# Kernel tuning notes

Hardware: AMD Instinct MI355X
Metric: run time of the kernel (lower is better)

The kernel has to match this reference:

```python
import jax, jax.numpy as jnp
import numpy as np

B, N, D, H, IN, HID = 16, 1024, 256, 8, 256, 1024
HD = IN // H  # head dim = 32
EPS = 1e-5


def layer_norm(x, g, b):
    mu = jnp.mean(x, axis=-1, keepdims=True)
    var = jnp.var(x, axis=-1, keepdims=True)
    return (x - mu) / jnp.sqrt(var + EPS) * g + b


def setup_inputs() -> dict:
    key = jax.random.key(0)
    ks = jax.random.split(key, 12)
    s = 0.02
    return {
        "x": jax.random.normal(ks[0], (B, N, D), jnp.float32),
        "coords": jax.random.normal(ks[1], (B, N, 2), jnp.float32),
        "g1": jnp.ones((D,), jnp.float32),
        "b1": jnp.zeros((D,), jnp.float32),
        "Wqkv": jax.random.normal(ks[2], (3 * IN, D), jnp.float32) * s,
        "Wproj": jax.random.normal(ks[3], (IN, IN), jnp.float32) * s,
        "bproj": jnp.zeros((IN,), jnp.float32),
        "g2": jnp.ones((D,), jnp.float32),
        "b2": jnp.zeros((D,), jnp.float32),
        "W1": jax.random.normal(ks[4], (HID, D), jnp.float32) * s,
        "bb1": jnp.zeros((HID,), jnp.float32),
        "W2": jax.random.normal(ks[5], (D, HID), jnp.float32) * s,
        "bb2": jnp.zeros((D,), jnp.float32),
    }


def reference(x, coords, g1, b1, Wqkv, Wproj, bproj, g2, b2, W1, bb1, W2, bb2):
    # ---- Attention branch (pre-norm) ----
    h = layer_norm(x, g1, b1)                       # [B,N,D]
    qkv = h @ Wqkv.T                                # [B,N,3*IN]
    qkv = qkv.reshape(B, N, 3, H, HD).transpose(2, 0, 3, 1, 4)  # [3,B,H,N,HD]
    q, k, v = qkv[0], qkv[1], qkv[2]
    scale = HD ** -0.5
    attn = jnp.einsum('bhid,bhjd->bhij', q * scale, k)  # [B,H,N,N]
    attn = jax.nn.softmax(attn, axis=-1)
    o = jnp.einsum('bhij,bhjd->bhid', attn, v)      # [B,H,N,HD]
    o = o.transpose(0, 2, 1, 3).reshape(B, N, IN)   # [B,N,IN]
    o = o @ Wproj.T + bproj
    o = o + h                                       # residual inside Attention (vs normed input)
    x = x + o                                       # Block residual (double residual, faithful)
    # ---- MLP branch ----
    h2 = layer_norm(x, g2, b2)
    m = jax.nn.gelu(h2 @ W1.T + bb1, approximate=False) @ W2.T + bb2
    return x + m
```

## Files before the change

kernel.cpp:

```cpp
#include <hip/hip_runtime.h>
#include <hip/hip_bf16.h>
#include <math.h>

#define Bdim 16
#define Ndim 1024
#define Ddim 256
#define Hdim 8
#define HDdim 32
#define INdim 256
#define HIDdim 1024
#define Tdim (Bdim * Ndim)

typedef __attribute__((ext_vector_type(8)))  short bf16x8;
typedef __attribute__((ext_vector_type(4)))  short bf16x4;
typedef __attribute__((ext_vector_type(16))) float f32x16;
typedef unsigned int u32;

__device__ inline short f2bf(float x) {
    union { __hip_bfloat16 b; short s; } u;
    u.b = __float2bfloat16(x);
    return u.s;
}

__device__ inline float bf2f(short s) {
    return __uint_as_float(((u32)(unsigned short)s) << 16);
}

__device__ inline float fexp2(float x) {
#if __has_builtin(__builtin_amdgcn_exp2f)
    return __builtin_amdgcn_exp2f(x);
#else
    return exp2f(x);
#endif
}

__device__ inline u32 pack2bf(float a, float b) {
#if __has_builtin(__builtin_amdgcn_cvt_pk_bf16_f32)
    typedef __attribute__((ext_vector_type(2))) __bf16 bf16x2_t;
    union { bf16x2_t v; u32 u; } c;
    c.v = __builtin_amdgcn_cvt_pk_bf16_f32(a, b);
    return c.u;
#else
    u32 ua = __float_as_uint(a), ub = __float_as_uint(b);
    return ((ua + 0x8000u) >> 16) | ((ub + 0x8000u) & 0xffff0000u);
#endif
}

__device__ inline void plswap(u32 &a, u32 &b) {
    asm volatile("v_permlane32_swap_b32 %0, %1" : "+v"(a), "+v"(b));
}

__device__ inline float gelu_exact(float v) {
    return 0.5f * v * (1.0f + erff(v * 0.70710678118654752f));
}

typedef __attribute__((address_space(1))) const u32 gas_t;
typedef __attribute__((address_space(3))) u32 las_t;
__device__ inline void gl16(const short* g, short* l) {
    __builtin_amdgcn_global_load_lds((gas_t*)g, (las_t*)l, 16, 0, 0);
}

#define N4_QKV  (3 * INdim * Ddim / 4)
#define N4_PROJ (INdim * INdim / 4)
#define N4_W1   (HIDdim * Ddim / 4)
#define N4_W2   (Ddim * HIDdim / 4)
#define NCVT_BLK ((N4_QKV + N4_PROJ + N4_W1 + N4_W2) / 256)

__global__ __launch_bounds__(256) void cvt_ln1_kernel(const float* __restrict__ s0,
                                                      const float* __restrict__ s1,
                                                      const float* __restrict__ s2,
                                                      const float* __restrict__ s3,
                                                      short* __restrict__ d0,
                                                      short* __restrict__ d1,
                                                      short* __restrict__ d2,
                                                      short* __restrict__ d3,
                                                      const float* __restrict__ x,
                                                      const float* __restrict__ g,
                                                      const float* __restrict__ b,
                                                      float* __restrict__ outf,
                                                      short* __restrict__ outb) {
    const int bid = blockIdx.x;
    if (bid < NCVT_BLK) {
        int i = bid * 256 + threadIdx.x;
        const float* src; short* dst; int j;
        if (i < N4_QKV)                          { src = s0; dst = d0; j = i; }
        else if (i < N4_QKV + N4_PROJ)           { src = s1; dst = d1; j = i - N4_QKV; }
        else if (i < N4_QKV + N4_PROJ + N4_W1)   { src = s2; dst = d2; j = i - N4_QKV - N4_PROJ; }
        else                                     { src = s3; dst = d3; j = i - N4_QKV - N4_PROJ - N4_W1; }
        float4 v = ((const float4*)src)[j];
        bf16x4 bb;
        bb[0] = f2bf(v.x); bb[1] = f2bf(v.y); bb[2] = f2bf(v.z); bb[3] = f2bf(v.w);
        ((bf16x4*)dst)[j] = bb;
    } else {
        int w = threadIdx.x >> 6, lane = threadIdx.x & 63;
        int row = (bid - NCVT_BLK) * 4 + w;
        float4 v = ((const float4*)x)[(size_t)row * 64 + lane];
        float s  = (v.x + v.y) + (v.z + v.w);
        float s2 = (v.x * v.x + v.y * v.y) + (v.z * v.z + v.w * v.w);
        #pragma unroll
        for (int off = 32; off; off >>= 1) {
            s  += __shfl_xor(s,  off, 64);
            s2 += __shfl_xor(s2, off, 64);
        }
        float mu   = s * (1.0f / Ddim);
        float var  = s2 * (1.0f / Ddim) - mu * mu;
        float rstd = rsqrtf(var + 1e-5f);
        float4 gg = ((const float4*)g)[lane];
        float4 bb = ((const float4*)b)[lane];
        float4 r;
        r.x = (v.x - mu) * rstd * gg.x + bb.x;
        r.y = (v.y - mu) * rstd * gg.y + bb.y;
        r.z = (v.z - mu) * rstd * gg.z + bb.z;
        r.w = (v.w - mu) * rstd * gg.w + bb.w;
        if (outf) ((float4*)outf)[(size_t)row * 64 + lane] = r;
        bf16x4 rb;
        rb[0] = f2bf(r.x); rb[1] = f2bf(r.y); rb[2] = f2bf(r.z); rb[3] = f2bf(r.w);
        ((bf16x4*)outb)[(size_t)row * 64 + lane] = rb;
    }
}

__global__ __launch_bounds__(256) void ln4_kernel(const float* __restrict__ x,
                                                  const float* __restrict__ g,
                                                  const float* __restrict__ b,
                                                  float* __restrict__ outf,
                                                  short* __restrict__ outb) {
    int w = threadIdx.x >> 6, lane = threadIdx.x & 63;
    int row = blockIdx.x * 4 + w;
    float4 v = ((const float4*)x)[(size_t)row * 64 + lane];
    float s  = (v.x + v.y) + (v.z + v.w);
    float s2 = (v.x * v.x + v.y * v.y) + (v.z * v.z + v.w * v.w);
    #pragma unroll
    for (int off = 32; off; off >>= 1) {
        s  += __shfl_xor(s,  off, 64);
        s2 += __shfl_xor(s2, off, 64);
    }
    float mu   = s * (1.0f / Ddim);
    float var  = s2 * (1.0f / Ddim) - mu * mu;
    float rstd = rsqrtf(var + 1e-5f);
    float4 gg = ((const float4*)g)[lane];
    float4 bb = ((const float4*)b)[lane];
    float4 r;
    r.x = (v.x - mu) * rstd * gg.x + bb.x;
    r.y = (v.y - mu) * rstd * gg.y + bb.y;
    r.z = (v.z - mu) * rstd * gg.z + bb.z;
    r.w = (v.w - mu) * rstd * gg.w + bb.w;
    if (outf) ((float4*)outf)[(size_t)row * 64 + lane] = r;
    bf16x4 rb;
    rb[0] = f2bf(r.x); rb[1] = f2bf(r.y); rb[2] = f2bf(r.z); rb[3] = f2bf(r.w);
    ((bf16x4*)outb)[(size_t)row * 64 + lane] = rb;
}

#define EPI_NONE 0
#define EPI_PROJ 1
#define EPI_GELU 2
#define EPI_RES  3
#define EPI_QKV  4

#define SCALE2Q 0.25505654249892417f

template <int EPI>
__global__ __launch_bounds__(256) void gemm128p(const short* __restrict__ A,
                                                const short* __restrict__ W,
                                                short* __restrict__ C,
                                                int N, int K,
                                                const float* __restrict__ bias) {
    __shared__ __attribute__((aligned(16))) short As[2][128 * 64];
    __shared__ __attribute__((aligned(16))) short Bs[2][128 * 64];
    const int tid = threadIdx.x, w = tid >> 6, lane = tid & 63;
    const int col = lane & 31;
    const int half_id = lane >> 5;

    const int nbx = gridDim.x;
    const int flat = blockIdx.y * nbx + blockIdx.x;
    const int cpx = (nbx * (int)gridDim.y) >> 3;
    const int swz = (flat & 7) * cpx + (flat >> 3);
    const int m0 = (swz / nbx) * 128, n0 = (swz % nbx) * 128;

    const int wm = (w & 1) * 64;
    const int wn = (w >> 1) * 64;

    f32x16 acc[2][2];
    #pragma unroll
    for (int i = 0; i < 2; ++i) { acc[i][0] = 0.0f; acc[i][1] = 0.0f; }

    const int lrow = lane >> 3;
    const int lchk = (lane & 7) ^ lrow;
    const short* gA = &A[(size_t)(m0 + w * 32 + lrow) * K + lchk * 8];
    const short* gB = &W[(size_t)(n0 + w * 32 + lrow) * K + lchk * 8];

    const int T = K >> 6;

    auto STAGE = [&](int buf, int kt) {
        short* lA = &As[buf][(w * 32) * 64];
        short* lB = &Bs[buf][(w * 32) * 64];
        #pragma unroll
        for (int i = 0; i < 4; ++i) {
            gl16(gA + (size_t)(i * 8) * K + kt * 64, lA + i * 512);
            gl16(gB + (size_t)(i * 8) * K + kt * 64, lB + i * 512);
        }
    };

    STAGE(0, 0);
    if (T > 1) {
        STAGE(1, 1);
        asm volatile("s_waitcnt vmcnt(8)" ::: "memory");
    } else {
        asm volatile("s_waitcnt vmcnt(0)" ::: "memory");
    }
    __builtin_amdgcn_s_barrier();

    for (int kt = 0; kt < T; ++kt) {
        const int buf = kt & 1;
        #pragma unroll
        for (int ks = 0; ks < 4; ++ks) {
            const int c = ks * 2 + half_id;
            bf16x8 af[2], bfv[2];
            #pragma unroll
            for (int t = 0; t < 2; ++t) {
                const int Ra = wm + t * 32 + col;
                af[t] = *(const bf16x8*)&As[buf][Ra * 64 + ((c ^ (Ra & 7)) * 8)];
                const int Rb = wn + t * 32 + col;
                bfv[t] = *(const bf16x8*)&Bs[buf][Rb * 64 + ((c ^ (Rb & 7)) * 8)];
            }
            #pragma unroll
            for (int tm = 0; tm < 2; ++tm)
                #pragma unroll
                for (int tn = 0; tn < 2; ++tn)
                    acc[tm][tn] = __builtin_amdgcn_mfma_f32_32x32x16_bf16(
                        af[tm], bfv[tn], acc[tm][tn], 0, 0, 0);
        }
        asm volatile("s_waitcnt lgkmcnt(0)" ::: "memory");
        __builtin_amdgcn_s_barrier();
        if (kt + 2 < T) {
            STAGE(buf, kt + 2);
            asm volatile("s_waitcnt vmcnt(8)" ::: "memory");
        } else {
            asm volatile("s_waitcnt vmcnt(0)" ::: "memory");
        }
        __builtin_amdgcn_s_barrier();
    }

    #pragma unroll
    for (int tm = 0; tm < 2; ++tm) {
        #pragma unroll
        for (int r = 0; r < 16; ++r) {
            int row = m0 + wm + tm * 32 + (r & 3) + 8 * (r >> 2) + 4 * half_id;
            #pragma unroll
            for (int tn = 0; tn < 2; ++tn) {
                int cn = n0 + wn + tn * 32 + col;
                float v = acc[tm][tn][r];
                if (EPI == EPI_QKV && cn < 256) v *= SCALE2Q;
                if (EPI == EPI_GELU) v = gelu_exact(v + bias[cn]);
                C[(size_t)row * N + cn] = f2bf(v);
            }
        }
    }
}

#define GPAD32 40

__device__ inline bf16x8 comb8(bf16x8 a, bf16x8 b, float rl) {
    bf16x8 r;
    #pragma unroll
    for (int i = 0; i < 8; ++i) r[i] = f2bf((bf2f(a[i]) + bf2f(b[i])) * rl);
    return r;
}

template <int EPI, int BN, bool COMB>
__global__ __launch_bounds__(256) void gemm_mfma(const short* __restrict__ A,
                                                 const short* __restrict__ W,
                                                 void* __restrict__ Cv,
                                                 int M, int N, int K,
                                                 const float* __restrict__ bias,
                                                 const float* __restrict__ add1,
                                                 const float* __restrict__ add2,
                                                 const float* __restrict__ lpc) {
    __shared__ short As[64 * GPAD32];
    __shared__ short Bs[BN * GPAD32];
    const int tid = threadIdx.x, w = tid >> 6, lane = tid & 63;
    const int col = lane & 31;
    const int half_id = lane >> 5;

    const int nbx = gridDim.x;
    const int flat = blockIdx.y * nbx + blockIdx.x;
    const int cpx = (nbx * (int)gridDim.y) >> 3;
    const int swz = (flat & 7) * cpx + (flat >> 3);
    const int m0 = (swz / nbx) * 64, n0 = (swz % nbx) * BN;

    const int wm = (w & 1) * 32;
    const int wn = (BN == 128) ? (w >> 1) * 64 : (w >> 1) * 32;
    constexpr int TN = (BN == 128) ? 2 : 1;

    f32x16 acc[TN];
    #pragma unroll
    for (int t = 0; t < TN; ++t) acc[t] = 0.0f;

    const int sra = tid >> 2, ssa = (tid & 3) * 8;
    const int srb = (BN == 128) ? (tid >> 1) : (tid >> 2);
    const int ssb = (BN == 128) ? (tid & 1) * 16 : (tid & 3) * 8;
    constexpr int NB = (BN == 128) ? 2 : 1;

    const short* pAsrc = &A[(size_t)(m0 + sra) * K + ssa];
    const short* pBsrc = &W[(size_t)(n0 + srb) * K + ssb];
    const float* lpr0 = COMB ? (lpc + (size_t)(m0 + sra) * 8) : nullptr;
    const float* lpr1 = COMB ? (lpr0 + (size_t)Tdim * 8) : nullptr;

    bf16x8 pa, pa2, pb[NB];
    float pl = 0.0f;
    pa = *(const bf16x8*)&pAsrc[0];
    if constexpr (COMB) {
        pa2 = *(const bf16x8*)(pAsrc + (size_t)Tdim * 256);
        pl = lpr0[0] + lpr1[0];
    }
    #pragma unroll
    for (int j = 0; j < NB; ++j) pb[j] = *(const bf16x8*)&pBsrc[j * 8];

    const int T = K >> 5;
    for (int kt = 0; kt < T; ++kt) {
        __syncthreads();
        {
            bf16x8 av = pa;
            if constexpr (COMB) av = comb8(pa, pa2, 1.0f / pl);
            *(bf16x8*)&As[sra * GPAD32 + ssa] = av;
        }
        #pragma unroll
        for (int j = 0; j < NB; ++j) *(bf16x8*)&Bs[srb * GPAD32 + ssb + j * 8] = pb[j];
        __syncthreads();

        if (kt + 1 < T) {
            const short* a = pAsrc + (kt + 1) * 32;
            const short* b = pBsrc + (kt + 1) * 32;
            pa = *(const bf16x8*)&a[0];
            if constexpr (COMB) {
                pa2 = *(const bf16x8*)(a + (size_t)Tdim * 256);
                pl = lpr0[kt + 1] + lpr1[kt + 1];
            }
            #pragma unroll
            for (int j = 0; j < NB; ++j) pb[j] = *(const bf16x8*)&b[j * 8];
        }

        #pragma unroll
        for (int ks = 0; ks < 2; ++ks) {
            bf16x8 af = *(const bf16x8*)&As[(wm + col) * GPAD32 + ks * 16 + half_id * 8];
            bf16x8 bfv[TN];
            #pragma unroll
            for (int t = 0; t < TN; ++t)
                bfv[t] = *(const bf16x8*)&Bs[(wn + t * 32 + col) * GPAD32 + ks * 16 + half_id * 8];
            #pragma unroll
            for (int t = 0; t < TN; ++t)
                acc[t] = __builtin_amdgcn_mfma_f32_32x32x16_bf16(af, bfv[t], acc[t], 0, 0, 0);
        }
    }

    float* Cf = (float*)Cv;
    short* Cb = (short*)Cv;
    #pragma unroll
    for (int r = 0; r < 16; ++r) {
        int row = m0 + wm + (r & 3) + 8 * (r >> 2) + 4 * half_id;
        #pragma unroll
        for (int t = 0; t < TN; ++t) {
            int cn = n0 + wn + t * 32 + col;
            size_t off = (size_t)row * N + cn;
            float v = acc[t][r];
            if (EPI != EPI_NONE && EPI != EPI_QKV) v += bias[cn];
            if (EPI == EPI_GELU) v = gelu_exact(v);
            if (EPI == EPI_PROJ) v += add1[off] + add2[off];
            if (EPI == EPI_RES)  v += add1[off];
            if (EPI == EPI_PROJ || EPI == EPI_RES) Cf[off] = v;
            else                                   Cb[off] = f2bf(v);
        }
    }
}

#define VTPAD 136

__global__ __launch_bounds__(256) void vtrans_kernel(const short* __restrict__ qkv,
                                                     short* __restrict__ vT) {
    __shared__ short Tl[32 * VTPAD];
    const int tid = threadIdx.x;
    const int bh = blockIdx.x, c = blockIdx.y;
    const int b = bh >> 3, head = bh & 7;
    {
        int r = tid >> 1, hv = tid & 1;
        const short* src = qkv + (size_t)b * Ndim * 768 + (size_t)(c * 128 + r) * 768
                           + 512 + head * 32 + hv * 16;
        bf16x8 v0 = *(const bf16x8*)&src[0];
        bf16x8 v1 = *(const bf16x8*)&src[8];
        #pragma unroll
        for (int i = 0; i < 8; ++i) {
            Tl[(hv * 16 + i) * VTPAD + r]     = v0[i];
            Tl[(hv * 16 + 8 + i) * VTPAD + r] = v1[i];
        }
    }
    __syncthreads();
    {
        int d = tid >> 3, j16 = (tid & 7) * 16;
        short* dst = vT + (size_t)(bh * 32 + d) * Ndim + c * 128 + j16;
        *(bf16x8*)&dst[0] = *(const bf16x8*)&Tl[d * VTPAD + j16];
        *(bf16x8*)&dst[8] = *(const bf16x8*)&Tl[d * VTPAD + j16 + 8];
    }
}

#define KVPAD 40
#define CHUNK 128

__global__ __launch_bounds__(256) void attn_mfma_kernel(const short* __restrict__ qkv,
                                                        const short* __restrict__ vT,
                                                        short* __restrict__ opart,
                                                        float* __restrict__ lpart) {
    __shared__ short Ks[CHUNK * KVPAD];
    __shared__ short Vt[32 * VTPAD];

    const int tid = threadIdx.x;
    const int w = tid >> 6;
    const int lane = tid & 63;
    const int col = lane & 31;
    const int half_id = lane >> 5;

    const int id = blockIdx.x;
    const int xcd = id & 7;
    const int s_ = id >> 3;
    const int bh = ((s_ >> 4) << 3) | xcd;
    const int qp = s_ & 15;
    const int qblk = qp & 7;
    const int part = qp >> 3;

    const int b = bh >> 3, head = bh & 7;
    const int q0w = qblk * 128 + w * 32;

    const size_t qkvb = (size_t)b * Ndim * 768;
    short* op = opart + (size_t)part * Tdim * 256;
    float* lp = lpart + (size_t)part * Tdim * 8;

    const int sr = tid >> 1, shv = tid & 1;
    const short* ksrc = qkv + qkvb + (size_t)sr * 768 + 256 + head * 32 + shv * 16;
    const int sd = tid >> 3, sj16 = (tid & 7) * 16;
    const short* vsrc = vT + (size_t)(bh * 32 + sd) * Ndim + sj16;

    bf16x8 qf[2];
    {
        const short* qrow = qkv + qkvb + (size_t)(q0w + col) * 768 + head * 32;
        #pragma unroll
        for (int kh = 0; kh < 2; ++kh)
            qf[kh] = *(const bf16x8*)&qrow[kh * 16 + half_id * 8];
    }

    bf16x8 vone;
    #pragma unroll
    for (int i = 0; i < 8; ++i) vone[i] = (short)0x3F80;

    f32x16 o_acc = 0.0f, l_acc = 0.0f;

    const int c0 = part * 4;

    bf16x8 rk0, rk1, rv0, rv1;
    {
        const short* kp = ksrc + (size_t)(c0 * CHUNK) * 768;
        rk0 = *(const bf16x8*)&kp[0];
        rk1 = *(const bf16x8*)&kp[8];
        const short* vp = vsrc + c0 * CHUNK;
        rv0 = *(const bf16x8*)&vp[0];
        rv1 = *(const bf16x8*)&vp[8];
    }

    #pragma unroll
    for (int ci = 0; ci < 4; ++ci) {
        if (ci != 0) __syncthreads();
        *(bf16x8*)&Ks[sr * KVPAD + shv * 16]     = rk0;
        *(bf16x8*)&Ks[sr * KVPAD + shv * 16 + 8] = rk1;
        *(bf16x8*)&Vt[sd * VTPAD + sj16]     = rv0;
        *(bf16x8*)&Vt[sd * VTPAD + sj16 + 8] = rv1;
        __syncthreads();

        if (ci < 3) {
            const short* kp = ksrc + (size_t)((c0 + ci + 1) * CHUNK) * 768;
            rk0 = *(const bf16x8*)&kp[0];
            rk1 = *(const bf16x8*)&kp[8];
            const short* vp = vsrc + (c0 + ci + 1) * CHUNK;
            rv0 = *(const bf16x8*)&vp[0];
            rv1 = *(const bf16x8*)&vp[8];
        }

        f32x16 s_cur;
        {
            bf16x8 kf0 = *(bf16x8*)&Ks[col * KVPAD + half_id * 8];
            bf16x8 kf1 = *(bf16x8*)&Ks[col * KVPAD + 16 + half_id * 8];
            f32x16 z = 0.0f;
            z = __builtin_amdgcn_mfma_f32_32x32x16_bf16(kf0, qf[0], z, 0, 0, 0);
            z = __builtin_amdgcn_mfma_f32_32x32x16_bf16(kf1, qf[1], z, 0, 0, 0);
            s_cur = z;
        }
        #pragma unroll
        for (int jt = 0; jt < 4; ++jt) {
            f32x16 s_next;
            if (jt < 3) {
                bf16x8 kf0 = *(bf16x8*)&Ks[((jt + 1) * 32 + col) * KVPAD + half_id * 8];
                bf16x8 kf1 = *(bf16x8*)&Ks[((jt + 1) * 32 + col) * KVPAD + 16 + half_id * 8];
                f32x16 z = 0.0f;
                z = __builtin_amdgcn_mfma_f32_32x32x16_bf16(kf0, qf[0], z, 0, 0, 0);
                z = __builtin_amdgcn_mfma_f32_32x32x16_bf16(kf1, qf[1], z, 0, 0, 0);
                s_next = z;
            }

            bf16x8 vf0 = *(bf16x8*)&Vt[col * VTPAD + jt * 32 + half_id * 8];
            bf16x8 vf1 = *(bf16x8*)&Vt[col * VTPAD + jt * 32 + 16 + half_id * 8];

            u32 wd[8];
            #pragma unroll
            for (int g = 0; g < 8; ++g) {
                float e0 = fexp2(s_cur[2 * g + 0]);
                float e1 = fexp2(s_cur[2 * g + 1]);
                wd[g] = pack2bf(e0, e1);
            }
            plswap(wd[0], wd[2]); plswap(wd[1], wd[3]);
            plswap(wd[4], wd[6]); plswap(wd[5], wd[7]);

            union { u32 u[4]; bf16x8 v; } p0, p1;
            p0.u[0] = wd[0]; p0.u[1] = wd[1]; p0.u[2] = wd[2]; p0.u[3] = wd[3];
            p1.u[0] = wd[4]; p1.u[1] = wd[5]; p1.u[2] = wd[6]; p1.u[3] = wd[7];

            __builtin_amdgcn_s_setprio(1);
            o_acc = __builtin_amdgcn_mfma_f32_32x32x16_bf16(p0.v, vf0, o_acc, 0, 0, 0);
            o_acc = __builtin_amdgcn_mfma_f32_32x32x16_bf16(p1.v, vf1, o_acc, 0, 0, 0);
            l_acc = __builtin_amdgcn_mfma_f32_32x32x16_bf16(p0.v, vone, l_acc, 0, 0, 0);
            l_acc = __builtin_amdgcn_mfma_f32_32x32x16_bf16(p1.v, vone, l_acc, 0, 0, 0);
            __builtin_amdgcn_s_setprio(0);

            if (jt < 3) s_cur = s_next;
        }
    }

    #pragma unroll
    for (int r = 0; r < 16; ++r) {
        int q_r = (r & 3) + 8 * (r >> 2) + 4 * half_id;
        size_t gq = (size_t)(b * Ndim + q0w + q_r);
        op[gq * INdim + head * 32 + col] = f2bf(o_acc[r]);
    }
    if (col < 16) {
        int r = col;
        int q_r = (r & 3) + 8 * (r >> 2) + 4 * half_id;
        lp[(size_t)(b * Ndim + q0w + q_r) * 8 + head] = l_acc[r];
    }
}

extern "C" void kernel_launch(void* const* d_in, const int* in_sizes, int n_in,
                              void* d_out, int out_size, void* d_ws, size_t ws_size,
                              hipStream_t stream) {
    const float* x     = (const float*)d_in[0];
    const float* g1    = (const float*)d_in[2];
    const float* b1    = (const float*)d_in[3];
    const float* Wqkv  = (const float*)d_in[4];
    const float* Wproj = (const float*)d_in[5];
    const float* bproj = (const float*)d_in[6];
    const float* g2    = (const float*)d_in[7];
    const float* b2    = (const float*)d_in[8];
    const float* W1    = (const float*)d_in[9];
    const float* bb1   = (const float*)d_in[10];
    const float* W2    = (const float*)d_in[11];
    const float* bb2   = (const float*)d_in[12];
    float* out = (float*)d_out;

    char* ws = (char*)d_ws;
    float* h      = (float*)(ws);
    short* h_bf   = (short*)(ws + (size_t)(16u << 20));
    short* qkv_bf = (short*)(ws + (size_t)(24u << 20));
    float* xnew   = (float*)(ws + (size_t)(24u << 20));
    short* opart  = (short*)(ws + (size_t)(48u << 20));
    short* mid_bf = (short*)(ws + (size_t)(48u << 20));
    float* lpart  = (float*)(ws + (size_t)(80u << 20));
    short* vT     = (short*)(ws + (size_t)(81u << 20));
    short* wqkv_b = (short*)(ws + (size_t)(89u << 20));
    short* wproj_b= (short*)(ws + (size_t)(89u << 20) + 768 * 1024);
    short* w1_b   = (short*)(ws + (size_t)(90u << 20));
    short* w2_b   = (short*)(ws + (size_t)(90u << 20) + 512 * 1024);

    cvt_ln1_kernel<<<NCVT_BLK + Tdim / 4, 256, 0, stream>>>(
        Wqkv, Wproj, W1, W2, wqkv_b, wproj_b, w1_b, w2_b,
        x, g1, b1, h, h_bf);
    gemm128p<EPI_QKV><<<dim3(768 / 128, Tdim / 128), 256, 0, stream>>>(
        h_bf, wqkv_b, qkv_bf, 768, 256, nullptr);
    vtrans_kernel<<<dim3(Bdim * Hdim, Ndim / 128), 256, 0, stream>>>(qkv_bf, vT);
    attn_mfma_kernel<<<2048, 256, 0, stream>>>(qkv_bf, vT, opart, lpart);
    gemm_mfma<EPI_PROJ, 64, true><<<dim3(256 / 64, Tdim / 64), 256, 0, stream>>>(
        opart, wproj_b, xnew, Tdim, 256, 256, bproj, h, x, lpart);
    ln4_kernel<<<Tdim / 4, 256, 0, stream>>>(xnew, g2, b2, nullptr, h_bf);
    gemm128p<EPI_GELU><<<dim3(1024 / 128, Tdim / 128), 256, 0, stream>>>(
        h_bf, w1_b, mid_bf, 1024, 256, bb1);
    gemm_mfma<EPI_RES, 64, false><<<dim3(256 / 64, Tdim / 64), 256, 0, stream>>>(
        mid_bf, w2_b, out, Tdim, 256, 1024, bb2, xnew, nullptr, nullptr);
}
```

Baseline: 212.4 us.

## Drop split-KV attention; each block processes full key range and normalizes in-kernel

```diff
diff --git a/kernel.cpp b/kernel.cpp
--- a/kernel.cpp
+++ b/kernel.cpp
@@ -259,22 +259,14 @@
 
 #define GPAD32 40
 
-__device__ inline bf16x8 comb8(bf16x8 a, bf16x8 b, float rl) {
-    bf16x8 r;
-    #pragma unroll
-    for (int i = 0; i < 8; ++i) r[i] = f2bf((bf2f(a[i]) + bf2f(b[i])) * rl);
-    return r;
-}
-
-template <int EPI, int BN, bool COMB>
+template <int EPI, int BN>
 __global__ __launch_bounds__(256) void gemm_mfma(const short* __restrict__ A,
                                                  const short* __restrict__ W,
                                                  void* __restrict__ Cv,
                                                  int M, int N, int K,
                                                  const float* __restrict__ bias,
                                                  const float* __restrict__ add1,
-                                                 const float* __restrict__ add2,
-                                                 const float* __restrict__ lpc) {
+                                                 const float* __restrict__ add2) {
     __shared__ short As[64 * GPAD32];
     __shared__ short Bs[BN * GPAD32];
     const int tid = threadIdx.x, w = tid >> 6, lane = tid & 63;
@@ -302,27 +294,16 @@
 
     const short* pAsrc = &A[(size_t)(m0 + sra) * K + ssa];
     const short* pBsrc = &W[(size_t)(n0 + srb) * K + ssb];
-    const float* lpr0 = COMB ? (lpc + (size_t)(m0 + sra) * 8) : nullptr;
-    const float* lpr1 = COMB ? (lpr0 + (size_t)Tdim * 8) : nullptr;
-
-    bf16x8 pa, pa2, pb[NB];
-    float pl = 0.0f;
+
+    bf16x8 pa, pb[NB];
     pa = *(const bf16x8*)&pAsrc[0];
-    if constexpr (COMB) {
-        pa2 = *(const bf16x8*)(pAsrc + (size_t)Tdim * 256);
-        pl = lpr0[0] + lpr1[0];
-    }
     #pragma unroll
     for (int j = 0; j < NB; ++j) pb[j] = *(const bf16x8*)&pBsrc[j * 8];
 
     const int T = K >> 5;
     for (int kt = 0; kt < T; ++kt) {
         __syncthreads();
-        {
-            bf16x8 av = pa;
-            if constexpr (COMB) av = comb8(pa, pa2, 1.0f / pl);
-            *(bf16x8*)&As[sra * GPAD32 + ssa] = av;
-        }
+        *(bf16x8*)&As[sra * GPAD32 + ssa] = pa;
         #pragma unroll
         for (int j = 0; j < NB; ++j) *(bf16x8*)&Bs[srb * GPAD32 + ssb + j * 8] = pb[j];
         __syncthreads();
@@ -331,10 +312,6 @@
             const short* a = pAsrc + (kt + 1) * 32;
             const short* b = pBsrc + (kt + 1) * 32;
             pa = *(const bf16x8*)&a[0];
-            if constexpr (COMB) {
-                pa2 = *(const bf16x8*)(a + (size_t)Tdim * 256);
-                pl = lpr0[kt + 1] + lpr1[kt + 1];
-            }
             #pragma unroll
             for (int j = 0; j < NB; ++j) pb[j] = *(const bf16x8*)&b[j * 8];
         }
@@ -406,8 +383,7 @@
 
 __global__ __launch_bounds__(256) void attn_mfma_kernel(const short* __restrict__ qkv,
                                                         const short* __restrict__ vT,
-                                                        short* __restrict__ opart,
-                                                        float* __restrict__ lpart) {
+                                                        short* __restrict__ oat) {
     __shared__ short Ks[CHUNK * KVPAD];
     __shared__ short Vt[32 * VTPAD];
 
@@ -420,17 +396,13 @@
     const int id = blockIdx.x;
     const int xcd = id & 7;
     const int s_ = id >> 3;
-    const int bh = ((s_ >> 4) << 3) | xcd;
-    const int qp = s_ & 15;
-    const int qblk = qp & 7;
-    const int part = qp >> 3;
+    const int bh = ((s_ >> 3) << 3) | xcd;
+    const int qblk = s_ & 7;
 
     const int b = bh >> 3, head = bh & 7;
     const int q0w = qblk * 128 + w * 32;
 
     const size_t qkvb = (size_t)b * Ndim * 768;
-    short* op = opart + (size_t)part * Tdim * 256;
-    float* lp = lpart + (size_t)part * Tdim * 8;
 
     const int sr = tid >> 1, shv = tid & 1;
     const short* ksrc = qkv + qkvb + (size_t)sr * 768 + 256 + head * 32 + shv * 16;
@@ -451,20 +423,15 @@
 
     f32x16 o_acc = 0.0f, l_acc = 0.0f;
 
-    const int c0 = part * 4;
-
     bf16x8 rk0, rk1, rv0, rv1;
     {
-        const short* kp = ksrc + (size_t)(c0 * CHUNK) * 768;
-        rk0 = *(const bf16x8*)&kp[0];
-        rk1 = *(const bf16x8*)&kp[8];
-        const short* vp = vsrc + c0 * CHUNK;
-        rv0 = *(const bf16x8*)&vp[0];
-        rv1 = *(const bf16x8*)&vp[8];
-    }
-
-    #pragma unroll
-    for (int ci = 0; ci < 4; ++ci) {
+        rk0 = *(const bf16x8*)&ksrc[0];
+        rk1 = *(const bf16x8*)&ksrc[8];
+        rv0 = *(const bf16x8*)&vsrc[0];
+        rv1 = *(const bf16x8*)&vsrc[8];
+    }
+
+    for (int ci = 0; ci < 8; ++ci) {
         if (ci != 0) __syncthreads();
         *(bf16x8*)&Ks[sr * KVPAD + shv * 16]     = rk0;
         *(bf16x8*)&Ks[sr * KVPAD + shv * 16 + 8] = rk1;
@@ -472,11 +439,11 @@
         *(bf16x8*)&Vt[sd * VTPAD + sj16 + 8] = rv1;
         __syncthreads();
 
-        if (ci < 3) {
-            const short* kp = ksrc + (size_t)((c0 + ci + 1) * CHUNK) * 768;
+        if (ci < 7) {
+            const short* kp = ksrc + (size_t)((ci + 1) * CHUNK) * 768;
             rk0 = *(const bf16x8*)&kp[0];
             rk1 = *(const bf16x8*)&kp[8];
-            const short* vp = vsrc + (c0 + ci + 1) * CHUNK;
+            const short* vp = vsrc + (ci + 1) * CHUNK;
             rv0 = *(const bf16x8*)&vp[0];
             rv1 = *(const bf16x8*)&vp[8];
         }
@@ -534,12 +501,7 @@
     for (int r = 0; r < 16; ++r) {
         int q_r = (r & 3) + 8 * (r >> 2) + 4 * half_id;
         size_t gq = (size_t)(b * Ndim + q0w + q_r);
-        op[gq * INdim + head * 32 + col] = f2bf(o_acc[r]);
-    }
-    if (col < 16) {
-        int r = col;
-        int q_r = (r & 3) + 8 * (r >> 2) + 4 * half_id;
-        lp[(size_t)(b * Ndim + q0w + q_r) * 8 + head] = l_acc[r];
+        oat[gq * INdim + head * 32 + col] = f2bf(o_acc[r] / l_acc[r]);
     }
 }
 
@@ -565,9 +527,8 @@
     short* h_bf   = (short*)(ws + (size_t)(16u << 20));
     short* qkv_bf = (short*)(ws + (size_t)(24u << 20));
     float* xnew   = (float*)(ws + (size_t)(24u << 20));
-    short* opart  = (short*)(ws + (size_t)(48u << 20));
-    short* mid_bf = (short*)(ws + (size_t)(48u << 20));
-    float* lpart  = (float*)(ws + (size_t)(80u << 20));
+    short* oat_bf = (short*)(ws + (size_t)(48u << 20));
+    short* mid_bf = (short*)(ws + (size_t)(56u << 20));
     short* vT     = (short*)(ws + (size_t)(81u << 20));
     short* wqkv_b = (short*)(ws + (size_t)(89u << 20));
     short* wproj_b= (short*)(ws + (size_t)(89u << 20) + 768 * 1024);
@@ -580,12 +541,12 @@
     gemm128p<EPI_QKV><<<dim3(768 / 128, Tdim / 128), 256, 0, stream>>>(
         h_bf, wqkv_b, qkv_bf, 768, 256, nullptr);
     vtrans_kernel<<<dim3(Bdim * Hdim, Ndim / 128), 256, 0, stream>>>(qkv_bf, vT);
-    attn_mfma_kernel<<<2048, 256, 0, stream>>>(qkv_bf, vT, opart, lpart);
-    gemm_mfma<EPI_PROJ, 64, true><<<dim3(256 / 64, Tdim / 64), 256, 0, stream>>>(
-        opart, wproj_b, xnew, Tdim, 256, 256, bproj, h, x, lpart);
+    attn_mfma_kernel<<<1024, 256, 0, stream>>>(qkv_bf, vT, oat_bf);
+    gemm_mfma<EPI_PROJ, 64><<<dim3(256 / 64, Tdim / 64), 256, 0, stream>>>(
+        oat_bf, wproj_b, xnew, Tdim, 256, 256, bproj, h, x);
     ln4_kernel<<<Tdim / 4, 256, 0, stream>>>(xnew, g2, b2, nullptr, h_bf);
     gemm128p<EPI_GELU><<<dim3(1024 / 128, Tdim / 128), 256, 0, stream>>>(
         h_bf, w1_b, mid_bf, 1024, 256, bb1);
-    gemm_mfma<EPI_RES, 64, false><<<dim3(256 / 64, Tdim / 64), 256, 0, stream>>>(
-        mid_bf, w2_b, out, Tdim, 256, 1024, bb2, xnew, nullptr, nullptr);
-}
+    gemm_mfma<EPI_RES, 64><<<dim3(256 / 64, Tdim / 64), 256, 0, stream>>>(
+        mid_bf, w2_b, out, Tdim, 256, 1024, bb2, xnew, nullptr);
+}
```

Result: faster. 208.0 us (-2.1%).
